# Optimization experiments

Hardware: AMD Instinct MI355X
Metric: run time of the kernel (lower is better)

The kernel has to match this reference:

```python
import jax, jax.numpy as jnp
import numpy as np

DIM_IN = 256
DIM_H = 64


def setup_inputs() -> dict:
    key = jax.random.key(0)
    ks = jax.random.split(key, 7)
    s = 1.0 / np.sqrt(DIM_IN + DIM_H)  # torch Linear default init scale
    inp = {
        "inputs": jax.random.normal(ks[0], (256, 512, DIM_IN), dtype=jnp.float32),
        # weights stored as (in_features, out_features) for x @ W
        "W_input": jax.random.uniform(ks[1], (DIM_IN + DIM_H, DIM_H), minval=-s, maxval=s, dtype=jnp.float32),
        "b_input": jax.random.uniform(ks[2], (DIM_H,), minval=-s, maxval=s, dtype=jnp.float32),
        "W_update": jax.random.uniform(ks[3], (DIM_IN + DIM_H, DIM_H), minval=-s, maxval=s, dtype=jnp.float32),
        "b_update": jax.random.uniform(ks[4], (DIM_H,), minval=-s, maxval=s, dtype=jnp.float32),
        "W_reset": jax.random.uniform(ks[5], (DIM_IN + DIM_H, DIM_H), minval=-s, maxval=s, dtype=jnp.float32),
        "b_reset": jax.random.uniform(ks[6], (DIM_H,), minval=-s, maxval=s, dtype=jnp.float32),
    }
    return inp


def reference(inputs, W_input, b_input, W_update, b_update, W_reset, b_reset):
    batch = inputs.shape[0]

    # Split each (dim_in+H, H) weight into its input-part and hidden-part so we
    # avoid per-step concatenation: cat([x, h]) @ W == x @ Wx + h @ Wh.
    Wi_x, Wi_h = W_input[:DIM_IN], W_input[DIM_IN:]
    Wu_x, Wu_h = W_update[:DIM_IN], W_update[DIM_IN:]
    Wr_x, Wr_h = W_reset[:DIM_IN], W_reset[DIM_IN:]

    # Precompute all input-side projections in one big GEMM: [B, L, H]
    xu = jnp.einsum('bld,dh->blh', inputs, Wu_x) + b_update
    xr = jnp.einsum('bld,dh->blh', inputs, Wr_x) + b_reset
    xi = jnp.einsum('bld,dh->blh', inputs, Wi_x) + b_input

    def step(h_prev, xs):
        xu_t, xr_t, xi_t = xs  # each [B, H]
        z = jax.nn.sigmoid(xu_t + h_prev @ Wu_h)
        r = jax.nn.sigmoid(xr_t + h_prev @ Wr_h)
        h_next = (1.0 - z) * h_prev + z * jnp.tanh(xi_t + (h_prev * r) @ Wi_h)
        return h_next, h_next

    h0 = jnp.zeros((batch, DIM_H), dtype=inputs.dtype)
    xs = (jnp.swapaxes(xu, 0, 1), jnp.swapaxes(xr, 0, 1), jnp.swapaxes(xi, 0, 1))  # [L, B, H]
    _, outs = jax.lax.scan(step, h0, xs)
    return jnp.swapaxes(outs, 0, 1)  # [B, L, H]
```

## Files before the change

kernel.cpp:

```cpp
#include <hip/hip_runtime.h>

#define DIM_IN 256
#define DIM_H 64
#define SEQ_LEN 512

typedef _Float16 h2_t  __attribute__((ext_vector_type(2)));
typedef _Float16 h8_t  __attribute__((ext_vector_type(8)));
typedef float    f32x4 __attribute__((ext_vector_type(4)));
union H8 { h8_t v; h2_t p[4]; };

typedef const __attribute__((address_space(1))) unsigned* gcu32_p;
typedef const __attribute__((address_space(1))) _Float16* gch16_p;
typedef const __attribute__((address_space(1))) float*    gcf32_p;
typedef       __attribute__((address_space(1))) float*    gf32_p;

__device__ inline float dot2(h2_t a, h2_t b, float c) {
#if __has_builtin(__builtin_amdgcn_fdot2)
    return __builtin_amdgcn_fdot2(a, b, c, false);
#else
    return c + (float)a[0] * (float)b[0] + (float)a[1] * (float)b[1];
#endif
}
__device__ inline float sigmoid_(float x) { return __fdividef(1.f, 1.f + __expf(-x)); }
__device__ inline float tanh_(float x)    { return 1.f - 2.f * __fdividef(1.f, 1.f + __expf(2.f * x)); }

#define LDS_FENCE() __asm__ volatile("s_waitcnt lgkmcnt(0)" ::: "memory")

template <int XI16>
__global__ __launch_bounds__(256, 1)
void gru_prepass_mfma(const float* __restrict__ X,
                      const float* __restrict__ W_input,  const float* __restrict__ b_input,
                      const float* __restrict__ W_update, const float* __restrict__ b_update,
                      const float* __restrict__ W_reset,  const float* __restrict__ b_reset,
                      unsigned* __restrict__ xur_out,
                      _Float16* __restrict__ xi16_out, float* __restrict__ xi32_out)
{
    const int tid  = threadIdx.x;
    const int lane = tid & 63;
    const int wv   = tid >> 6;
    const int q    = lane >> 4;
    const int m16  = lane & 15;

    constexpr int LDK = DIM_IN + 8;
    __shared__ _Float16 xs[64 * LDK];

    const int c = wv * 16 + m16;
    h8_t bu[8], brf[8], bif[8];
#pragma unroll
    for (int kt = 0; kt < 8; ++kt) {
        h8_t u, r, i;
#pragma unroll
        for (int jj = 0; jj < 8; ++jj) {
            const int k = kt * 32 + q * 8 + jj;
            u[jj] = (_Float16)W_update[k * DIM_H + c];
            r[jj] = (_Float16)W_reset [k * DIM_H + c];
            i[jj] = (_Float16)W_input [k * DIM_H + c];
        }
        bu[kt] = u; brf[kt] = r; bif[kt] = i;
    }
    const float bzc = b_update[c], brc = b_reset[c], bic = b_input[c];

    const float4* xblk = (const float4*)(X + (size_t)blockIdx.x * 64 * DIM_IN);
#pragma unroll
    for (int i = 0; i < 16; ++i) {
        const int f   = tid + 256 * i;
        const int row = f >> 6;
        const int kq  = f & 63;
        const float4 v = xblk[f];
        h2_t a, b;
        a[0] = (_Float16)v.x; a[1] = (_Float16)v.y;
        b[0] = (_Float16)v.z; b[1] = (_Float16)v.w;
        _Float16* dst = &xs[row * LDK + kq * 4];
        *(h2_t*)dst = a; *(h2_t*)(dst + 2) = b;
    }
    __syncthreads();

    const size_t orow0 = (size_t)blockIdx.x * 64;
#pragma unroll
    for (int rt = 0; rt < 4; ++rt) {
        const int r0 = rt * 16;
        f32x4 au = {0.f,0.f,0.f,0.f}, ar = {0.f,0.f,0.f,0.f}, ai = {0.f,0.f,0.f,0.f};
#pragma unroll
        for (int kt = 0; kt < 8; ++kt) {
            const h8_t a = *(const h8_t*)&xs[(r0 + m16) * LDK + kt * 32 + q * 8];
            au = __builtin_amdgcn_mfma_f32_16x16x32_f16(a, bu[kt],  au, 0, 0, 0);
            ar = __builtin_amdgcn_mfma_f32_16x16x32_f16(a, brf[kt], ar, 0, 0, 0);
            ai = __builtin_amdgcn_mfma_f32_16x16x32_f16(a, bif[kt], ai, 0, 0, 0);
        }
#pragma unroll
        for (int i = 0; i < 4; ++i) {
            const size_t grow = orow0 + r0 + q * 4 + i;
            h2_t pk;
            pk[0] = (_Float16)(au[i] + bzc);
            pk[1] = (_Float16)(ar[i] + brc);
            xur_out[grow * DIM_H + c] = __builtin_bit_cast(unsigned, pk);
            const float xiv = ai[i] + bic;
            if (XI16) xi16_out[grow * DIM_H + c] = (_Float16)xiv;
            else      xi32_out[grow * DIM_H + c] = xiv;
        }
    }
}

template <int XI16>
__global__ __launch_bounds__(64, 1)
void gru_rec(const unsigned* __restrict__ xur, const _Float16* __restrict__ xi16,
             const float* __restrict__ W_input, const float* __restrict__ W_update,
             const float* __restrict__ W_reset,
             float* __restrict__ out)
{
    const int b = blockIdx.x;
    const int j = threadIdx.x;

    __shared__ __align__(16) _Float16 hh[DIM_H];
    __shared__ __align__(16) _Float16 ss[DIM_H];

    h2_t wu[32], wr[32], wi[32];
#pragma unroll
    for (int m = 0; m < 32; ++m) {
        const int k = DIM_IN + 2 * m;
        h2_t a, cc, d;
        a[0]  = (_Float16)W_update[(k    ) * DIM_H + j];
        a[1]  = (_Float16)W_update[(k + 1) * DIM_H + j];
        cc[0] = (_Float16)W_reset [(k    ) * DIM_H + j];
        cc[1] = (_Float16)W_reset [(k + 1) * DIM_H + j];
        d[0]  = (_Float16)W_input [(k    ) * DIM_H + j];
        d[1]  = (_Float16)W_input [(k + 1) * DIM_H + j];
        wu[m] = a; wr[m] = cc; wi[m] = d;
    }

    hh[j] = (_Float16)0.f;
    float hprev = 0.f;

    const size_t base = (size_t)b * SEQ_LEN * DIM_H + j;
    gcu32_p xg  = (gcu32_p)(xur + base);
    gch16_p ig  = (gch16_p)(xi16 + base);
    gcf32_p xog = (gcf32_p)(out + base);
    gf32_p  og  = (gf32_p)(out + base);

    unsigned ru[8];
    float    rxi[8];
#pragma unroll
    for (int d = 0; d < 8; ++d) {
        ru[d]  = xg[(size_t)d * DIM_H];
        rxi[d] = XI16 ? (float)ig[(size_t)d * DIM_H] : xog[(size_t)d * DIM_H];
    }
    LDS_FENCE();

    for (int tb = 0; tb < SEQ_LEN / 8; ++tb) {
#pragma unroll
        for (int u = 0; u < 8; ++u) {
            const int t = tb * 8 + u;
            const h2_t pr = __builtin_bit_cast(h2_t, ru[u]);
            const float xu = (float)pr[0];
            const float xr = (float)pr[1];
            const float xi = rxi[u];
            const int tp = (t + 8 < SEQ_LEN) ? t + 8 : SEQ_LEN - 1;
            ru[u]  = xg[(size_t)tp * DIM_H];
            rxi[u] = XI16 ? (float)ig[(size_t)tp * DIM_H] : xog[(size_t)tp * DIM_H];

            const H8* hp = (const H8*)hh;
            float az0=0,az1=0,az2=0,az3=0, ar0=0,ar1=0,ar2=0,ar3=0;
#pragma unroll
            for (int qq = 0; qq < 8; ++qq) {
                H8 hx; hx.v = hp[qq].v;
                az0 = dot2(hx.p[0], wu[4*qq+0], az0);
                ar0 = dot2(hx.p[0], wr[4*qq+0], ar0);
                az1 = dot2(hx.p[1], wu[4*qq+1], az1);
                ar1 = dot2(hx.p[1], wr[4*qq+1], ar1);
                az2 = dot2(hx.p[2], wu[4*qq+2], az2);
                ar2 = dot2(hx.p[2], wr[4*qq+2], ar2);
                az3 = dot2(hx.p[3], wu[4*qq+3], az3);
                ar3 = dot2(hx.p[3], wr[4*qq+3], ar3);
            }
            const float z = sigmoid_(xu + ((az0 + az1) + (az2 + az3)));
            const float r = sigmoid_(xr + ((ar0 + ar1) + (ar2 + ar3)));

            ss[j] = (_Float16)(hprev * r);
            LDS_FENCE();

            const H8* sp = (const H8*)ss;
            float ax0=0,ax1=0,ax2=0,ax3=0;
#pragma unroll
            for (int qq = 0; qq < 8; ++qq) {
                H8 sx; sx.v = sp[qq].v;
                ax0 = dot2(sx.p[0], wi[4*qq+0], ax0);
                ax1 = dot2(sx.p[1], wi[4*qq+1], ax1);
                ax2 = dot2(sx.p[2], wi[4*qq+2], ax2);
                ax3 = dot2(sx.p[3], wi[4*qq+3], ax3);
            }
            const float th = tanh_(xi + ((ax0 + ax1) + (ax2 + ax3)));
            const float hn = (1.f - z) * hprev + z * th;

            og[(size_t)t * DIM_H] = hn;
            hh[j] = (_Float16)hn;
            LDS_FENCE();
            hprev = hn;
        }
    }
}

extern "C" void kernel_launch(void* const* d_in, const int* in_sizes, int n_in,
                              void* d_out, int out_size, void* d_ws, size_t ws_size,
                              hipStream_t stream) {
    const float* inputs   = (const float*)d_in[0];
    const float* W_input  = (const float*)d_in[1];
    const float* b_input  = (const float*)d_in[2];
    const float* W_update = (const float*)d_in[3];
    const float* b_update = (const float*)d_in[4];
    const float* W_reset  = (const float*)d_in[5];
    const float* b_reset  = (const float*)d_in[6];
    float* out = (float*)d_out;

    const int    batch = in_sizes[0] / (SEQ_LEN * DIM_IN);
    const size_t rows  = (size_t)batch * SEQ_LEN;

    unsigned* xur_w = (unsigned*)d_ws;
    _Float16* xi_w  = (_Float16*)(xur_w + rows * DIM_H);
    const bool xi16 = ws_size >= rows * DIM_H * 6ull;

    if (xi16) {
        gru_prepass_mfma<1><<<(int)(rows / 64), 256, 0, stream>>>(
            inputs, W_input, b_input, W_update, b_update, W_reset, b_reset,
            xur_w, xi_w, out);
        gru_rec<1><<<batch, 64, 0, stream>>>(xur_w, xi_w,
                                             W_input, W_update, W_reset, out);
    } else {
        gru_prepass_mfma<0><<<(int)(rows / 64), 256, 0, stream>>>(
            inputs, W_input, b_input, W_update, b_update, W_reset, b_reset,
            xur_w, xi_w, out);
        gru_rec<0><<<batch, 64, 0, stream>>>(xur_w, xi_w,
                                             W_input, W_update, W_reset, out);
    }
}
```

Baseline: 479.4 us.

## Prescale activations, reorder gate dot products, and multi-tile prepass with prefetch

The prepass now folds the log2(e) scaling for sigmoid and tanh into the stored projections, so the recurrent kernel can use raw exp2 and rcp intrinsics instead of exp plus divide. Each prepass block handles four row tiles and prefetches the next tile into registers while the current one runs its MFMAs, with occupancy raised to 2. In the recurrence, the reset gate is computed first so the s=h*r store and barrier happen earlier, and the update-gate dot products move after that barrier to overlap with the wait. The output store is placed after the LDS fence. The risk is fp16 rounding of the prescaled values and higher register pressure.

```diff
diff --git a/kernel.cpp b/kernel.cpp
--- a/kernel.cpp
+++ b/kernel.cpp
@@ -1,8 +1,9 @@
 #include <hip/hip_runtime.h>
 
 #define DIM_IN 256
-#define DIM_H 64
+#define DIM_H  64
 #define SEQ_LEN 512
+#define TPB 4
 
 typedef _Float16 h2_t  __attribute__((ext_vector_type(2)));
 typedef _Float16 h8_t  __attribute__((ext_vector_type(8)));
@@ -21,13 +22,25 @@
     return c + (float)a[0] * (float)b[0] + (float)a[1] * (float)b[1];
 #endif
 }
-__device__ inline float sigmoid_(float x) { return __fdividef(1.f, 1.f + __expf(-x)); }
-__device__ inline float tanh_(float x)    { return 1.f - 2.f * __fdividef(1.f, 1.f + __expf(2.f * x)); }
+__device__ inline float exp2_(float x) {
+#if __has_builtin(__builtin_amdgcn_exp2f)
+    return __builtin_amdgcn_exp2f(x);
+#else
+    return exp2f(x);
+#endif
+}
+__device__ inline float rcp_(float x) {
+#if __has_builtin(__builtin_amdgcn_rcpf)
+    return __builtin_amdgcn_rcpf(x);
+#else
+    return __fdividef(1.f, x);
+#endif
+}
 
 #define LDS_FENCE() __asm__ volatile("s_waitcnt lgkmcnt(0)" ::: "memory")
 
 template <int XI16>
-__global__ __launch_bounds__(256, 1)
+__global__ __launch_bounds__(256, 2)
 void gru_prepass_mfma(const float* __restrict__ X,
                       const float* __restrict__ W_input,  const float* __restrict__ b_input,
                       const float* __restrict__ W_update, const float* __restrict__ b_update,
@@ -60,50 +73,87 @@
     }
     const float bzc = b_update[c], brc = b_reset[c], bic = b_input[c];
 
-    const float4* xblk = (const float4*)(X + (size_t)blockIdx.x * 64 * DIM_IN);
-#pragma unroll
-    for (int i = 0; i < 16; ++i) {
-        const int f   = tid + 256 * i;
-        const int row = f >> 6;
-        const int kq  = f & 63;
-        const float4 v = xblk[f];
-        h2_t a, b;
-        a[0] = (_Float16)v.x; a[1] = (_Float16)v.y;
-        b[0] = (_Float16)v.z; b[1] = (_Float16)v.w;
-        _Float16* dst = &xs[row * LDK + kq * 4];
-        *(h2_t*)dst = a; *(h2_t*)(dst + 2) = b;
-    }
-    __syncthreads();
-
-    const size_t orow0 = (size_t)blockIdx.x * 64;
-#pragma unroll
-    for (int rt = 0; rt < 4; ++rt) {
-        const int r0 = rt * 16;
-        f32x4 au = {0.f,0.f,0.f,0.f}, ar = {0.f,0.f,0.f,0.f}, ai = {0.f,0.f,0.f,0.f};
-#pragma unroll
-        for (int kt = 0; kt < 8; ++kt) {
-            const h8_t a = *(const h8_t*)&xs[(r0 + m16) * LDK + kt * 32 + q * 8];
-            au = __builtin_amdgcn_mfma_f32_16x16x32_f16(a, bu[kt],  au, 0, 0, 0);
-            ar = __builtin_amdgcn_mfma_f32_16x16x32_f16(a, brf[kt], ar, 0, 0, 0);
-            ai = __builtin_amdgcn_mfma_f32_16x16x32_f16(a, bif[kt], ai, 0, 0, 0);
-        }
-#pragma unroll
-        for (int i = 0; i < 4; ++i) {
-            const size_t grow = orow0 + r0 + q * 4 + i;
-            h2_t pk;
-            pk[0] = (_Float16)(au[i] + bzc);
-            pk[1] = (_Float16)(ar[i] + brc);
-            xur_out[grow * DIM_H + c] = __builtin_bit_cast(unsigned, pk);
-            const float xiv = ai[i] + bic;
-            if (XI16) xi16_out[grow * DIM_H + c] = (_Float16)xiv;
-            else      xi32_out[grow * DIM_H + c] = xiv;
-        }
-    }
-}
+    const int tile0 = blockIdx.x * TPB;
+    float4 pf[16];
+    {
+        const float4* xb = (const float4*)(X + (size_t)tile0 * 64 * DIM_IN);
+#pragma unroll
+        for (int i = 0; i < 16; ++i) pf[i] = xb[tid + 256 * i];
+    }
+
+#pragma unroll 1
+    for (int tI = 0; tI < TPB; ++tI) {
+#pragma unroll
+        for (int i = 0; i < 16; ++i) {
+            const int f   = tid + 256 * i;
+            const int row = f >> 6;
+            const int kq  = f & 63;
+            const float4 v = pf[i];
+            h2_t a, b2;
+            a[0]  = (_Float16)v.x; a[1]  = (_Float16)v.y;
+            b2[0] = (_Float16)v.z; b2[1] = (_Float16)v.w;
+            _Float16* dst = &xs[row * LDK + kq * 4];
+            *(h2_t*)dst = a; *(h2_t*)(dst + 2) = b2;
+        }
+        __syncthreads();
+        if (tI + 1 < TPB) {
+            const float4* xb = (const float4*)(X + (size_t)(tile0 + tI + 1) * 64 * DIM_IN);
+#pragma unroll
+            for (int i = 0; i < 16; ++i) pf[i] = xb[tid + 256 * i];
+        }
+        const size_t orow0 = (size_t)(tile0 + tI) * 64;
+#pragma unroll
+        for (int rt = 0; rt < 4; ++rt) {
+            const int r0 = rt * 16;
+            f32x4 au = {0.f,0.f,0.f,0.f}, ar = {0.f,0.f,0.f,0.f}, aa = {0.f,0.f,0.f,0.f};
+#pragma unroll
+            for (int kt = 0; kt < 8; ++kt) {
+                const h8_t a = *(const h8_t*)&xs[(r0 + m16) * LDK + kt * 32 + q * 8];
+                au = __builtin_amdgcn_mfma_f32_16x16x32_f16(a, bu[kt],  au, 0, 0, 0);
+                ar = __builtin_amdgcn_mfma_f32_16x16x32_f16(a, brf[kt], ar, 0, 0, 0);
+                aa = __builtin_amdgcn_mfma_f32_16x16x32_f16(a, bif[kt], aa, 0, 0, 0);
+            }
+#pragma unroll
+            for (int i = 0; i < 4; ++i) {
+                const size_t grow = orow0 + r0 + q * 4 + i;
+                h2_t pk;
+                pk[0] = (_Float16)(-1.44269504f * (au[i] + bzc));
+                pk[1] = (_Float16)(-1.44269504f * (ar[i] + brc));
+                xur_out[grow * DIM_H + c] = __builtin_bit_cast(unsigned, pk);
+                const float xiv = 2.88539008f * (aa[i] + bic);
+                if (XI16) xi16_out[grow * DIM_H + c] = (_Float16)xiv;
+                else      xi32_out[grow * DIM_H + c] = xiv;
+            }
+        }
+        __syncthreads();
+    }
+}
+
+
+#define DOTR(HX, Q)                                                 \
+    ar0 = dot2(HX.p[0], wr[4*(Q)+0], ar0);                          \
+    ar1 = dot2(HX.p[1], wr[4*(Q)+1], ar1);                          \
+    ar2 = dot2(HX.p[2], wr[4*(Q)+2], ar2);                          \
+    ar3 = dot2(HX.p[3], wr[4*(Q)+3], ar3);
+
+#define DOTZ(HX, Q)                                                 \
+    az0 = dot2(HX.p[0], wu[4*(Q)+0], az0);                          \
+    az1 = dot2(HX.p[1], wu[4*(Q)+1], az1);                          \
+    az2 = dot2(HX.p[2], wu[4*(Q)+2], az2);                          \
+    az3 = dot2(HX.p[3], wu[4*(Q)+3], az3);
+
+#define DOTI(SX, Q)                                                 \
+    ax0 = dot2(SX.p[0], wi[4*(Q)+0], ax0);                          \
+    ax1 = dot2(SX.p[1], wi[4*(Q)+1], ax1);                          \
+    ax2 = dot2(SX.p[2], wi[4*(Q)+2], ax2);                          \
+    ax3 = dot2(SX.p[3], wi[4*(Q)+3], ax3);
 
 template <int XI16>
-__global__ __launch_bounds__(64, 1)
+__global__
+__attribute__((amdgpu_flat_work_group_size(64, 64)))
+__attribute__((amdgpu_waves_per_eu(1, 1)))
 void gru_rec(const unsigned* __restrict__ xur, const _Float16* __restrict__ xi16,
+             const float* __restrict__ xif,
              const float* __restrict__ W_input, const float* __restrict__ W_update,
              const float* __restrict__ W_reset,
              float* __restrict__ out)
@@ -134,7 +184,7 @@
     const size_t base = (size_t)b * SEQ_LEN * DIM_H + j;
     gcu32_p xg  = (gcu32_p)(xur + base);
     gch16_p ig  = (gch16_p)(xi16 + base);
-    gcf32_p xog = (gcf32_p)(out + base);
+    gcf32_p igf = (gcf32_p)(xif + base);
     gf32_p  og  = (gf32_p)(out + base);
 
     unsigned ru[8];
@@ -142,10 +192,11 @@
 #pragma unroll
     for (int d = 0; d < 8; ++d) {
         ru[d]  = xg[(size_t)d * DIM_H];
-        rxi[d] = XI16 ? (float)ig[(size_t)d * DIM_H] : xog[(size_t)d * DIM_H];
+        rxi[d] = XI16 ? (float)ig[(size_t)d * DIM_H] : igf[(size_t)d * DIM_H];
     }
     LDS_FENCE();
 
+#pragma unroll 1
     for (int tb = 0; tb < SEQ_LEN / 8; ++tb) {
 #pragma unroll
         for (int u = 0; u < 8; ++u) {
@@ -156,44 +207,40 @@
             const float xi = rxi[u];
             const int tp = (t + 8 < SEQ_LEN) ? t + 8 : SEQ_LEN - 1;
             ru[u]  = xg[(size_t)tp * DIM_H];
-            rxi[u] = XI16 ? (float)ig[(size_t)tp * DIM_H] : xog[(size_t)tp * DIM_H];
+            rxi[u] = XI16 ? (float)ig[(size_t)tp * DIM_H] : igf[(size_t)tp * DIM_H];
 
             const H8* hp = (const H8*)hh;
-            float az0=0,az1=0,az2=0,az3=0, ar0=0,ar1=0,ar2=0,ar3=0;
-#pragma unroll
-            for (int qq = 0; qq < 8; ++qq) {
-                H8 hx; hx.v = hp[qq].v;
-                az0 = dot2(hx.p[0], wu[4*qq+0], az0);
-                ar0 = dot2(hx.p[0], wr[4*qq+0], ar0);
-                az1 = dot2(hx.p[1], wu[4*qq+1], az1);
-                ar1 = dot2(hx.p[1], wr[4*qq+1], ar1);
-                az2 = dot2(hx.p[2], wu[4*qq+2], az2);
-                ar2 = dot2(hx.p[2], wr[4*qq+2], ar2);
-                az3 = dot2(hx.p[3], wu[4*qq+3], az3);
-                ar3 = dot2(hx.p[3], wr[4*qq+3], ar3);
-            }
-            const float z = sigmoid_(xu + ((az0 + az1) + (az2 + az3)));
-            const float r = sigmoid_(xr + ((ar0 + ar1) + (ar2 + ar3)));
-
-            ss[j] = (_Float16)(hprev * r);
+            H8 hx0 = hp[0], hx1 = hp[1], hx2 = hp[2], hx3 = hp[3],
+               hx4 = hp[4], hx5 = hp[5], hx6 = hp[6], hx7 = hp[7];
+
+            float ar0 = 0.f, ar1 = 0.f, ar2 = 0.f, ar3 = 0.f;
+            DOTR(hx0,0) DOTR(hx1,1) DOTR(hx2,2) DOTR(hx3,3)
+            DOTR(hx4,4) DOTR(hx5,5) DOTR(hx6,6) DOTR(hx7,7)
+            const float rg = rcp_(1.f + exp2_(
+                fmaf((ar0 + ar1) + (ar2 + ar3), -1.44269504f, xr)));
+            ss[j] = (_Float16)(hprev * rg);
             LDS_FENCE();
 
             const H8* sp = (const H8*)ss;
-            float ax0=0,ax1=0,ax2=0,ax3=0;
-#pragma unroll
-            for (int qq = 0; qq < 8; ++qq) {
-                H8 sx; sx.v = sp[qq].v;
-                ax0 = dot2(sx.p[0], wi[4*qq+0], ax0);
-                ax1 = dot2(sx.p[1], wi[4*qq+1], ax1);
-                ax2 = dot2(sx.p[2], wi[4*qq+2], ax2);
-                ax3 = dot2(sx.p[3], wi[4*qq+3], ax3);
-            }
-            const float th = tanh_(xi + ((ax0 + ax1) + (ax2 + ax3)));
-            const float hn = (1.f - z) * hprev + z * th;
-
-            og[(size_t)t * DIM_H] = hn;
+            H8 sx0 = sp[0], sx1 = sp[1], sx2 = sp[2], sx3 = sp[3],
+               sx4 = sp[4], sx5 = sp[5], sx6 = sp[6], sx7 = sp[7];
+
+            float az0 = 0.f, az1 = 0.f, az2 = 0.f, az3 = 0.f;
+            DOTZ(hx0,0) DOTZ(hx1,1) DOTZ(hx2,2) DOTZ(hx3,3)
+            DOTZ(hx4,4) DOTZ(hx5,5) DOTZ(hx6,6) DOTZ(hx7,7)
+            const float zg = rcp_(1.f + exp2_(
+                fmaf((az0 + az1) + (az2 + az3), -1.44269504f, xu)));
+
+            float ax0 = 0.f, ax1 = 0.f, ax2 = 0.f, ax3 = 0.f;
+            DOTI(sx0,0) DOTI(sx1,1) DOTI(sx2,2) DOTI(sx3,3)
+            DOTI(sx4,4) DOTI(sx5,5) DOTI(sx6,6) DOTI(sx7,7)
+            const float th = fmaf(-2.f, rcp_(1.f + exp2_(
+                fmaf((ax0 + ax1) + (ax2 + ax3), 2.88539008f, xi))), 1.f);
+
+            const float hn = fmaf(zg, th - hprev, hprev);
             hh[j] = (_Float16)hn;
             LDS_FENCE();
+            og[(size_t)t * DIM_H] = hn;
             hprev = hn;
         }
     }
@@ -213,22 +260,23 @@
 
     const int    batch = in_sizes[0] / (SEQ_LEN * DIM_IN);
     const size_t rows  = (size_t)batch * SEQ_LEN;
+    const int    nblk  = (int)(rows / 64 / TPB);
 
     unsigned* xur_w = (unsigned*)d_ws;
     _Float16* xi_w  = (_Float16*)(xur_w + rows * DIM_H);
     const bool xi16 = ws_size >= rows * DIM_H * 6ull;
 
     if (xi16) {
-        gru_prepass_mfma<1><<<(int)(rows / 64), 256, 0, stream>>>(
+        gru_prepass_mfma<1><<<nblk, 256, 0, stream>>>(
             inputs, W_input, b_input, W_update, b_update, W_reset, b_reset,
             xur_w, xi_w, out);
-        gru_rec<1><<<batch, 64, 0, stream>>>(xur_w, xi_w,
+        gru_rec<1><<<batch, 64, 0, stream>>>(xur_w, xi_w, out,
                                              W_input, W_update, W_reset, out);
     } else {
-        gru_prepass_mfma<0><<<(int)(rows / 64), 256, 0, stream>>>(
+        gru_prepass_mfma<0><<<nblk, 256, 0, stream>>>(
             inputs, W_input, b_input, W_update, b_update, W_reset, b_reset,
             xur_w, xi_w, out);
-        gru_rec<0><<<batch, 64, 0, stream>>>(xur_w, xi_w,
+        gru_rec<0><<<batch, 64, 0, stream>>>(xur_w, xi_w, out,
                                              W_input, W_update, W_reset, out);
     }
 }
```

After: 422.5 us. 11.9% less time.
